# Optimization experiments

Hardware: AMD Instinct MI355X
Metric: run time of the kernel (lower is better)

## Reference

```python
import jax, jax.numpy as jnp
import numpy as np

N_NODES = 50000
N_EDGES = 1600000
NUM_GRAPHS = 512
NEG_SLOPE = 0.2


def _glorot(key, shape):
    fan_in, fan_out = shape[0], shape[-1]
    lim = jnp.sqrt(6.0 / (fan_in + fan_out))
    return jax.random.uniform(key, shape, jnp.float32, -lim, lim)


def setup_inputs() -> dict:
    key = jax.random.key(0)
    ks = jax.random.split(key, 10)
    x = jax.random.normal(ks[0], (N_NODES, 133), jnp.float32)
    edge_index = jax.random.randint(ks[1], (2, N_EDGES), 0, N_NODES, jnp.int64)
    batch = jnp.sort(jax.random.randint(ks[2], (N_NODES,), 0, NUM_GRAPHS, jnp.int64))
    # conv1: GATConv(133 -> 8, heads=8, concat=True)
    W1 = _glorot(ks[3], (133, 64))
    att_src1 = _glorot(ks[4], (8, 8))   # [H, C]
    att_dst1 = _glorot(ks[5], (8, 8))
    b1 = jnp.zeros((64,), jnp.float32)
    # conv2: GATConv(64 -> 2, heads=1, concat=True)
    W2 = _glorot(ks[6], (64, 2))
    att_src2 = _glorot(ks[7], (1, 2))
    att_dst2 = _glorot(ks[8], (1, 2))
    b2 = jnp.zeros((2,), jnp.float32)
    return {"x": x, "edge_index": edge_index, "batch": batch,
            "W1": W1, "att_src1": att_src1, "att_dst1": att_dst1, "b1": b1,
            "W2": W2, "att_src2": att_src2, "att_dst2": att_dst2, "b2": b2}


def gat_conv(x, src, dst, W, att_src, att_dst, bias):
    """PyG GATConv (add_self_loops already applied via src/dst), concat=True, eval mode."""
    N = x.shape[0]
    H, C = att_src.shape
    h = (x @ W).reshape(N, H, C)                      # [N, H, C]
    a_src = jnp.sum(h * att_src[None], axis=-1)       # [N, H]
    a_dst = jnp.sum(h * att_dst[None], axis=-1)       # [N, H]
    e = a_src[src] + a_dst[dst]                       # [E, H]
    e = jnp.where(e > 0, e, NEG_SLOPE * e)            # leaky_relu
    # segment softmax over incoming edges of each dst node
    e_max = jax.ops.segment_max(e, dst, num_segments=N)  # [N, H]
    e_exp = jnp.exp(e - e_max[dst])
    denom = jax.ops.segment_sum(e_exp, dst, num_segments=N)
    alpha = e_exp / jnp.maximum(denom, 1e-16)[dst]    # [E, H]
    msg = h[src] * alpha[:, :, None]                  # [E, H, C]
    out = jax.ops.segment_sum(msg, dst, num_segments=N)  # [N, H, C]
    return out.reshape(N, H * C) + bias


def reference(x, edge_index, batch, W1, att_src1, att_dst1, b1, W2, att_src2, att_dst2, b2):
    N = x.shape[0]
    loops = jnp.arange(N, dtype=edge_index.dtype)
    src = jnp.concatenate([edge_index[0], loops])
    dst = jnp.concatenate([edge_index[1], loops])
    # dropout layers are identity in eval mode
    h = gat_conv(x, src, dst, W1, att_src1, att_dst1, b1)   # [N, 64]
    h = jax.nn.elu(h)
    h = gat_conv(h, src, dst, W2, att_src2, att_dst2, b2)   # [N, 2]
    out = jax.ops.segment_sum(h, batch, num_segments=NUM_GRAPHS)  # [G, 2]
    return out
```

## Files before the change

kernel.cpp:

```cpp
#include <hip/hip_runtime.h>
#include <hip/hip_fp16.h>

#define NN 50000
#define NE 1600000
#define NG 512
#define NEG 0.2f

#define NBKT 782
#define NSB 512
#define CHUNK 3125
#define CAP 3072
#define NSLOT 32
#define NBI 9

typedef _Float16 half8 __attribute__((ext_vector_type(8)));
typedef float f32x4 __attribute__((ext_vector_type(4)));


__global__ __launch_bounds__(256) void k_init_count(const float* __restrict__ W1,
                                                    _Float16* __restrict__ W1f,
                                                    float* __restrict__ out,
                                                    const int* __restrict__ ei,
                                                    int* __restrict__ cnt) {
    if (blockIdx.x < NBI) {
        int i = blockIdx.x * 256 + threadIdx.x;
        if (i < 1280) {
            int f = i >> 6, l = i & 63;
            int kt = f >> 2, ct = f & 3;
            int g = l >> 4, c16 = l & 15;
#pragma unroll
            for (int j = 0; j < 8; ++j) {
                int k = kt * 32 + g * 8 + j;
                float v = (k < 133) ? W1[k * 64 + ct * 16 + c16] : 0.f;
                W1f[i * 8 + j] = (_Float16)v;
            }
        } else if (i < 1280 + NG * 2) {
            out[i - 1280] = 0.f;
        }
    } else {
        __shared__ int hist[NBKT];
        const int t = threadIdx.x, blk = blockIdx.x - NBI;
        for (int i = t; i < NBKT; i += 256) hist[i] = 0;
        __syncthreads();
        const int estart = blk * CHUNK;
        for (int e = estart + t; e < estart + CHUNK; e += 256)
            atomicAdd(&hist[ei[NE + e] >> 6], 1);
        __syncthreads();
        for (int i = t; i < NBKT; i += 256) cnt[blk * NBKT + i] = hist[i];
    }
}

__global__ __launch_bounds__(256) void k_linmfma(const float* __restrict__ x,
                                                 const _Float16* __restrict__ W1f,
                                                 const float* __restrict__ attS,
                                                 const float* __restrict__ attD,
                                                 __half* __restrict__ h1h,
                                                 float* __restrict__ aS,
                                                 float* __restrict__ aD) {
    const int wid = (blockIdx.x * 256 + threadIdx.x) >> 6;
    const int nb  = wid * 16;
    if (nb >= NN) return;
    const int l   = threadIdx.x & 63;
    const int g   = l >> 4, c16 = l & 15;
    const long xbase = (long)(nb + c16) * 133;

    half8 bfr[5][4];
#pragma unroll
    for (int kt = 0; kt < 5; ++kt)
#pragma unroll
        for (int ct = 0; ct < 4; ++ct)
            bfr[kt][ct] = *reinterpret_cast<const half8*>(W1f + ((kt * 4 + ct) * 64 + l) * 8);

    f32x4 acc[4] = {{0.f,0.f,0.f,0.f},{0.f,0.f,0.f,0.f},{0.f,0.f,0.f,0.f},{0.f,0.f,0.f,0.f}};
#pragma unroll
    for (int kt = 0; kt < 5; ++kt) {
        half8 a;
#pragma unroll
        for (int i = 0; i < 8; ++i) {
            int k = kt * 32 + g * 8 + i;
            a[i] = (_Float16)((k < 133) ? x[xbase + k] : 0.f);
        }
#pragma unroll
        for (int ct = 0; ct < 4; ++ct)
            acc[ct] = __builtin_amdgcn_mfma_f32_16x16x32_f16(a, bfr[kt][ct], acc[ct], 0, 0, 0);
    }

#pragma unroll
    for (int ct = 0; ct < 4; ++ct) {
        const int col  = ct * 16 + c16;
        const int head = col >> 3;
        const float as_w = attS[head * 8 + (col & 7)];
        const float ad_w = attD[head * 8 + (col & 7)];
#pragma unroll
        for (int r = 0; r < 4; ++r) {
            const int n = nb + g * 4 + r;
            float v = acc[ct][r];
            h1h[n * 64 + col] = __float2half(v);
            float ps = v * as_w, pd = v * ad_w;
            ps += __shfl_xor(ps, 1, 64); pd += __shfl_xor(pd, 1, 64);
            ps += __shfl_xor(ps, 2, 64); pd += __shfl_xor(pd, 2, 64);
            ps += __shfl_xor(ps, 4, 64); pd += __shfl_xor(pd, 4, 64);
            if ((l & 7) == 0) {
                aS[n * 8 + head] = ps;
                aD[n * 8 + head] = pd;
            }
        }
    }
}

__global__ __launch_bounds__(512) void k_scan(const int* __restrict__ cnt,
                                              int* __restrict__ base,
                                              int* __restrict__ tot) {
    __shared__ int s[NSB];
    const int b = blockIdx.x, t = threadIdx.x;
    int v = cnt[t * NBKT + b];
    s[t] = v;
    __syncthreads();
    for (int o = 1; o < NSB; o <<= 1) {
        int u = (t >= o) ? s[t - o] : 0;
        __syncthreads();
        s[t] += u;
        __syncthreads();
    }
    base[t * NBKT + b] = s[t] - v;
    if (t == NSB - 1) tot[b] = s[t];
}

__global__ __launch_bounds__(256) void k_place(const int* __restrict__ ei,
                                               const int* __restrict__ base,
                                               unsigned* __restrict__ binned) {
    __shared__ int hist[NBKT];
    __shared__ int basel[NBKT];
    const int t = threadIdx.x, blk = blockIdx.x;
    for (int i = t; i < NBKT; i += 256) {
        hist[i]  = 0;
        basel[i] = base[blk * NBKT + i];
    }
    __syncthreads();
    const int estart = blk * CHUNK;
    for (int e = estart + t; e < estart + CHUNK; e += 256) {
        int s = ei[e];
        int d = ei[NE + e];
        int b = d >> 6;
        int r = atomicAdd(&hist[b], 1);
        int pos = basel[b] + r;
        if (pos < CAP) binned[b * CAP + pos] = ((unsigned)s << 6) | (unsigned)(d & 63);
    }
}

__global__ __launch_bounds__(256) void k_buildcsr(const unsigned* __restrict__ binned,
                                                  const int* __restrict__ tot,
                                                  int2* __restrict__ row_se,
                                                  unsigned short* __restrict__ csr) {
    __shared__ unsigned edg[CAP];
    __shared__ unsigned short csrl[CAP];
    __shared__ int deg[64], scn[64], cur[64];

    const int b = blockIdx.x, t = threadIdx.x;
    const int ebase = b * CAP;
    const int ecnt  = min(tot[b], CAP);
    const int nbase = b << 6;
    const int ncnt  = min(64, NN - nbase);

    for (int i = t; i < ecnt; i += 256) edg[i] = binned[ebase + i];
    if (t < 64) deg[t] = 0;
    __syncthreads();
    for (int i = t; i < ecnt; i += 256) atomicAdd(&deg[edg[i] & 63], 1);
    __syncthreads();
    if (t < 64) scn[t] = deg[t];
    __syncthreads();
    for (int o = 1; o < 64; o <<= 1) {
        int v = (t < 64 && t >= o) ? scn[t - o] : 0;
        __syncthreads();
        if (t < 64) scn[t] += v;
        __syncthreads();
    }
    if (t < 64) {
        cur[t] = scn[t] - deg[t];
        if (t < ncnt) row_se[nbase + t] = make_int2(ebase + scn[t] - deg[t], ebase + scn[t]);
    }
    __syncthreads();
    for (int i = t; i < ecnt; i += 256) {
        unsigned pk = edg[i];
        int pos = atomicAdd(&cur[pk & 63], 1);
        csrl[pos] = (unsigned short)(pk >> 6);
    }
    __syncthreads();
    for (int i = t; i < ecnt; i += 256) csr[ebase + i] = csrl[i];
}

__global__ __launch_bounds__(256) void k_gather1(const unsigned short* __restrict__ csr,
                                                 const int2* __restrict__ row_se,
                                                 const float* __restrict__ aS,
                                                 const float* __restrict__ aD,
                                                 const uint2* __restrict__ h1u2,
                                                 const float* __restrict__ b1,
                                                 const float* __restrict__ W2,
                                                 const float* __restrict__ attS2,
                                                 const float* __restrict__ attD2,
                                                 float4* __restrict__ node4) {
    __shared__ float exs[4][64 * 8];
    __shared__ int   svs[4][64];

    const int sub  = threadIdx.x >> 6;
    const int lane = threadIdx.x & 63;
    const int n    = (blockIdx.x * 256 + threadIdx.x) >> 6;
    const int hp   = lane & 7;
    const int ebl  = lane >> 3;
    const int grp  = lane >> 4;
    const int c4   = lane & 15;
    const int hq   = c4 >> 1;

    const float aDhp = aD[n * 8 + hp];
    const int2 se = row_se[n];
    const int e0 = se.x, e1 = se.y;

    float ax = 0.f, ay = 0.f, az = 0.f, aw = 0.f;
    float den = 0.f;
    for (int base = e0; base < e1; base += 64) {
        const int cnt = min(64, e1 - base);
        int sv = (base + lane < e1) ? (int)csr[base + lane] : n;
        svs[sub][lane] = sv;

        const int cnt16 = (cnt + 15) & ~15;
        const int p1n   = cnt16 >> 3;

        for (int p = 0; p < p1n; ++p) {
            int eb = p * 8 + ebl;
            int s  = svs[sub][eb];
            float ev = aS[s * 8 + hp] + aDhp;
            ev = fmaxf(ev, NEG * ev);
            float ex = __expf(ev);
            if (eb >= cnt) ex = 0.f;
            exs[sub][eb * 8 + hp] = ex;
            den += ex;
        }

        for (int eb = 0; eb < cnt16; eb += 16) {
#pragma unroll
            for (int k = 0; k < 16; k += 4) {
                int   e4 = eb + k + grp;
                int   s  = svs[sub][e4];
                float ex = exs[sub][e4 * 8 + hq];
                uint2 hv = h1u2[s * 16 + c4];
                const __half2 h01 = *reinterpret_cast<const __half2*>(&hv.x);
                const __half2 h23 = *reinterpret_cast<const __half2*>(&hv.y);
                ax = fmaf(ex, __half2float(__low2half(h01)),  ax);
                ay = fmaf(ex, __half2float(__high2half(h01)), ay);
                az = fmaf(ex, __half2float(__low2half(h23)),  az);
                aw = fmaf(ex, __half2float(__high2half(h23)), aw);
            }
        }
    }
    den += __shfl_xor(den, 8, 64);
    den += __shfl_xor(den, 16, 64);
    den += __shfl_xor(den, 32, 64);
    float ev_s = aS[n * 8 + hp] + aDhp;
    ev_s = fmaxf(ev_s, NEG * ev_s);
    float ex_self = __expf(ev_s);
    den += ex_self;

    ax += __shfl_xor(ax, 16, 64); ax += __shfl_xor(ax, 32, 64);
    ay += __shfl_xor(ay, 16, 64); ay += __shfl_xor(ay, 32, 64);
    az += __shfl_xor(az, 16, 64); az += __shfl_xor(az, 32, 64);
    aw += __shfl_xor(aw, 16, 64); aw += __shfl_xor(aw, 32, 64);

    float den_q = __shfl(den, hq, 64);
    float ex_sq = __shfl(ex_self, hq, 64);

    uint2 hvs = h1u2[n * 16 + c4];
    const __half2 s01 = *reinterpret_cast<const __half2*>(&hvs.x);
    const __half2 s23 = *reinterpret_cast<const __half2*>(&hvs.y);
    float inv = 1.f / fmaxf(den_q, 1e-16f);
    float4 bb = reinterpret_cast<const float4*>(b1)[c4];
    float v0 = fmaf(ex_sq, __half2float(__low2half(s01)),  ax) * inv + bb.x;
    float v1 = fmaf(ex_sq, __half2float(__high2half(s01)), ay) * inv + bb.y;
    float v2 = fmaf(ex_sq, __half2float(__low2half(s23)),  az) * inv + bb.z;
    float v3 = fmaf(ex_sq, __half2float(__high2half(s23)), aw) * inv + bb.w;
    v0 = v0 > 0.f ? v0 : (__expf(v0) - 1.f);
    v1 = v1 > 0.f ? v1 : (__expf(v1) - 1.f);
    v2 = v2 > 0.f ? v2 : (__expf(v2) - 1.f);
    v3 = v3 > 0.f ? v3 : (__expf(v3) - 1.f);

    float4 w01 = reinterpret_cast<const float4*>(W2)[c4 * 2];
    float4 w23 = reinterpret_cast<const float4*>(W2)[c4 * 2 + 1];
    float p0 = v0 * w01.x + v1 * w01.z + v2 * w23.x + v3 * w23.z;
    float p1 = v0 * w01.y + v1 * w01.w + v2 * w23.y + v3 * w23.w;
    p0 += __shfl_xor(p0, 1, 64);  p1 += __shfl_xor(p1, 1, 64);
    p0 += __shfl_xor(p0, 2, 64);  p1 += __shfl_xor(p1, 2, 64);
    p0 += __shfl_xor(p0, 4, 64);  p1 += __shfl_xor(p1, 4, 64);
    p0 += __shfl_xor(p0, 8, 64);  p1 += __shfl_xor(p1, 8, 64);
    if (lane == 0) {
        float s2 = p0 * attS2[0] + p1 * attS2[1];
        float d2 = p0 * attD2[0] + p1 * attD2[1];
        node4[n] = make_float4(p0, p1, s2, d2);
    }
}

__global__ __launch_bounds__(256) void k_gather2(const unsigned short* __restrict__ csr,
                                                 const int2* __restrict__ row_se,
                                                 const float4* __restrict__ node4,
                                                 const int* __restrict__ batch,
                                                 const float* __restrict__ b2,
                                                 float* __restrict__ out) {
    __shared__ float pool[NSLOT][2];
    __shared__ int gbase_s;
    const int t = threadIdx.x;
    const int n = blockIdx.x * 256 + t;

    if (t == 0) gbase_s = batch[blockIdx.x * 256];
    for (int i = t; i < NSLOT * 2; i += 256) (&pool[0][0])[i] = 0.f;
    __syncthreads();

    if (n < NN) {
        const float4 vn = node4[n];
        const float aDd = vn.w;

        float ev = vn.z + aDd;
        ev = fmaxf(ev, NEG * ev);
        float ex = __expf(ev);
        float den = ex, p0 = ex * vn.x, p1 = ex * vn.y;

        const int2 se = row_se[n];
#pragma unroll 4
        for (int e = se.x; e < se.y; ++e) {
            int s = csr[e];
            float4 vs = node4[s];
            float ev2 = vs.z + aDd;
            ev2 = fmaxf(ev2, NEG * ev2);
            float ex2 = __expf(ev2);
            den += ex2;
            p0 = fmaf(ex2, vs.x, p0);
            p1 = fmaf(ex2, vs.y, p1);
        }
        float inv = 1.f / fmaxf(den, 1e-16f);
        float v0 = p0 * inv + b2[0];
        float v1 = p1 * inv + b2[1];

        int g = batch[n];
        int slot = g - gbase_s;
        if (slot < NSLOT) {
            atomicAdd(&pool[slot][0], v0);
            atomicAdd(&pool[slot][1], v1);
        } else {
            atomicAdd(&out[g * 2 + 0], v0);
            atomicAdd(&out[g * 2 + 1], v1);
        }
    }
    __syncthreads();
    for (int i = t; i < NSLOT; i += 256) {
        float v0 = pool[i][0], v1 = pool[i][1];
        if (v0 != 0.f || v1 != 0.f) {
            int g = gbase_s + i;
            atomicAdd(&out[g * 2 + 0], v0);
            atomicAdd(&out[g * 2 + 1], v1);
        }
    }
}

extern "C" void kernel_launch(void* const* d_in, const int* in_sizes, int n_in,
                              void* d_out, int out_size, void* d_ws, size_t ws_size,
                              hipStream_t stream) {
    const float* x     = (const float*)d_in[0];
    const int*   ei    = (const int*)d_in[1];
    const int*   batch = (const int*)d_in[2];
    const float* W1    = (const float*)d_in[3];
    const float* attS1 = (const float*)d_in[4];
    const float* attD1 = (const float*)d_in[5];
    const float* b1    = (const float*)d_in[6];
    const float* W2    = (const float*)d_in[7];
    const float* attS2 = (const float*)d_in[8];
    const float* attD2 = (const float*)d_in[9];
    const float* b2    = (const float*)d_in[10];
    float* out = (float*)d_out;

    int* ws = (int*)d_ws;
    __half* h1h = (__half*)ws;
    uint2* h1u2 = (uint2*)ws;
    float* aS1 = (float*)(ws + (size_t)NN * 32);
    float* aD1 = (float*)(ws + (size_t)NN * 40);
    float4* node4 = (float4*)(ws + (size_t)NN * 48);
    int2* row_se  = (int2*)(ws + (size_t)NN * 52);
    int* tot      = ws + (size_t)NN * 54;
    _Float16* W1f = (_Float16*)(ws + (size_t)NN * 54 + 1024);
    int* cnt      = ws + (size_t)NN * 55;
    int* base     = ws + (size_t)NN * 55 + (size_t)NSB * NBKT;
    unsigned* binned    = (unsigned*)(ws + (size_t)NN * 55 + 2 * (size_t)NSB * NBKT);
    unsigned short* csr = (unsigned short*)(binned + (size_t)NBKT * CAP);

    k_init_count<<<NBI + NSB, 256, 0, stream>>>(W1, W1f, out, ei, cnt);
    k_linmfma<<<(NN / 16 + 3) / 4, 256, 0, stream>>>(x, W1f, attS1, attD1, h1h, aS1, aD1);
    k_scan<<<NBKT, NSB, 0, stream>>>(cnt, base, tot);
    k_place<<<NSB, 256, 0, stream>>>(ei, base, binned);
    k_buildcsr<<<NBKT, 256, 0, stream>>>(binned, tot, row_se, csr);
    k_gather1<<<NN / 4, 256, 0, stream>>>(csr, row_se, aS1, aD1, h1u2, b1, W2,
                                          attS2, attD2, node4);
    k_gather2<<<(NN + 255) / 256, 256, 0, stream>>>(csr, row_se, node4, batch, b2, out);
}
```

Baseline: 109.5 us.

## Store layer-1 features as FP8 and merge the linear and edge-placement kernels

```diff
diff --git a/kernel.cpp b/kernel.cpp
--- a/kernel.cpp
+++ b/kernel.cpp
@@ -12,9 +12,11 @@
 #define CAP 3072
 #define NSLOT 32
 #define NBI 9
+#define NBL 782
 
 typedef _Float16 half8 __attribute__((ext_vector_type(8)));
 typedef float f32x4 __attribute__((ext_vector_type(4)));
+typedef float f32x2 __attribute__((ext_vector_type(2)));
 
 
 __global__ __launch_bounds__(256) void k_init_count(const float* __restrict__ W1,
@@ -50,64 +52,6 @@
     }
 }
 
-__global__ __launch_bounds__(256) void k_linmfma(const float* __restrict__ x,
-                                                 const _Float16* __restrict__ W1f,
-                                                 const float* __restrict__ attS,
-                                                 const float* __restrict__ attD,
-                                                 __half* __restrict__ h1h,
-                                                 float* __restrict__ aS,
-                                                 float* __restrict__ aD) {
-    const int wid = (blockIdx.x * 256 + threadIdx.x) >> 6;
-    const int nb  = wid * 16;
-    if (nb >= NN) return;
-    const int l   = threadIdx.x & 63;
-    const int g   = l >> 4, c16 = l & 15;
-    const long xbase = (long)(nb + c16) * 133;
-
-    half8 bfr[5][4];
-#pragma unroll
-    for (int kt = 0; kt < 5; ++kt)
-#pragma unroll
-        for (int ct = 0; ct < 4; ++ct)
-            bfr[kt][ct] = *reinterpret_cast<const half8*>(W1f + ((kt * 4 + ct) * 64 + l) * 8);
-
-    f32x4 acc[4] = {{0.f,0.f,0.f,0.f},{0.f,0.f,0.f,0.f},{0.f,0.f,0.f,0.f},{0.f,0.f,0.f,0.f}};
-#pragma unroll
-    for (int kt = 0; kt < 5; ++kt) {
-        half8 a;
-#pragma unroll
-        for (int i = 0; i < 8; ++i) {
-            int k = kt * 32 + g * 8 + i;
-            a[i] = (_Float16)((k < 133) ? x[xbase + k] : 0.f);
-        }
-#pragma unroll
-        for (int ct = 0; ct < 4; ++ct)
-            acc[ct] = __builtin_amdgcn_mfma_f32_16x16x32_f16(a, bfr[kt][ct], acc[ct], 0, 0, 0);
-    }
-
-#pragma unroll
-    for (int ct = 0; ct < 4; ++ct) {
-        const int col  = ct * 16 + c16;
-        const int head = col >> 3;
-        const float as_w = attS[head * 8 + (col & 7)];
-        const float ad_w = attD[head * 8 + (col & 7)];
-#pragma unroll
-        for (int r = 0; r < 4; ++r) {
-            const int n = nb + g * 4 + r;
-            float v = acc[ct][r];
-            h1h[n * 64 + col] = __float2half(v);
-            float ps = v * as_w, pd = v * ad_w;
-            ps += __shfl_xor(ps, 1, 64); pd += __shfl_xor(pd, 1, 64);
-            ps += __shfl_xor(ps, 2, 64); pd += __shfl_xor(pd, 2, 64);
-            ps += __shfl_xor(ps, 4, 64); pd += __shfl_xor(pd, 4, 64);
-            if ((l & 7) == 0) {
-                aS[n * 8 + head] = ps;
-                aD[n * 8 + head] = pd;
-            }
-        }
-    }
-}
-
 __global__ __launch_bounds__(512) void k_scan(const int* __restrict__ cnt,
                                               int* __restrict__ base,
                                               int* __restrict__ tot) {
@@ -126,25 +70,85 @@
     if (t == NSB - 1) tot[b] = s[t];
 }
 
-__global__ __launch_bounds__(256) void k_place(const int* __restrict__ ei,
-                                               const int* __restrict__ base,
-                                               unsigned* __restrict__ binned) {
-    __shared__ int hist[NBKT];
-    __shared__ int basel[NBKT];
-    const int t = threadIdx.x, blk = blockIdx.x;
-    for (int i = t; i < NBKT; i += 256) {
-        hist[i]  = 0;
-        basel[i] = base[blk * NBKT + i];
-    }
-    __syncthreads();
-    const int estart = blk * CHUNK;
-    for (int e = estart + t; e < estart + CHUNK; e += 256) {
-        int s = ei[e];
-        int d = ei[NE + e];
-        int b = d >> 6;
-        int r = atomicAdd(&hist[b], 1);
-        int pos = basel[b] + r;
-        if (pos < CAP) binned[b * CAP + pos] = ((unsigned)s << 6) | (unsigned)(d & 63);
+__global__ __launch_bounds__(256) void k_lin_place(const float* __restrict__ x,
+                                                   const _Float16* __restrict__ W1f,
+                                                   const float* __restrict__ attS,
+                                                   const float* __restrict__ attD,
+                                                   unsigned char* __restrict__ h1b,
+                                                   float* __restrict__ aS,
+                                                   float* __restrict__ aD,
+                                                   const int* __restrict__ ei,
+                                                   const int* __restrict__ base,
+                                                   unsigned* __restrict__ binned) {
+    if (blockIdx.x < NBL) {
+        const int wid = (blockIdx.x * 256 + threadIdx.x) >> 6;
+        const int nb  = wid * 16;
+        if (nb >= NN) return;
+        const int l   = threadIdx.x & 63;
+        const int g   = l >> 4, c16 = l & 15;
+        const long xbase = (long)(nb + c16) * 133;
+
+        half8 bfr[5][4];
+#pragma unroll
+        for (int kt = 0; kt < 5; ++kt)
+#pragma unroll
+            for (int ct = 0; ct < 4; ++ct)
+                bfr[kt][ct] = *reinterpret_cast<const half8*>(W1f + ((kt * 4 + ct) * 64 + l) * 8);
+
+        f32x4 acc[4] = {{0.f,0.f,0.f,0.f},{0.f,0.f,0.f,0.f},{0.f,0.f,0.f,0.f},{0.f,0.f,0.f,0.f}};
+#pragma unroll
+        for (int kt = 0; kt < 5; ++kt) {
+            half8 a;
+#pragma unroll
+            for (int i = 0; i < 8; ++i) {
+                int k = kt * 32 + g * 8 + i;
+                a[i] = (_Float16)((k < 133) ? x[xbase + k] : 0.f);
+            }
+#pragma unroll
+            for (int ct = 0; ct < 4; ++ct)
+                acc[ct] = __builtin_amdgcn_mfma_f32_16x16x32_f16(a, bfr[kt][ct], acc[ct], 0, 0, 0);
+        }
+
+#pragma unroll
+        for (int ct = 0; ct < 4; ++ct) {
+            const int col  = ct * 16 + c16;
+            const int head = col >> 3;
+            const float as_w = attS[head * 8 + (col & 7)];
+            const float ad_w = attD[head * 8 + (col & 7)];
+#pragma unroll
+            for (int r = 0; r < 4; ++r) {
+                const int n = nb + g * 4 + r;
+                float v = acc[ct][r];
+                h1b[n * 64 + col] =
+                    (unsigned char)__builtin_amdgcn_cvt_pk_fp8_f32(v, v, 0, false);
+                float ps = v * as_w, pd = v * ad_w;
+                ps += __shfl_xor(ps, 1, 64); pd += __shfl_xor(pd, 1, 64);
+                ps += __shfl_xor(ps, 2, 64); pd += __shfl_xor(pd, 2, 64);
+                ps += __shfl_xor(ps, 4, 64); pd += __shfl_xor(pd, 4, 64);
+                if ((l & 7) == 0) {
+                    aS[n * 8 + head] = ps;
+                    aD[n * 8 + head] = pd;
+                }
+            }
+        }
+    } else {
+        __shared__ int hist[NBKT];
+        __shared__ int basel[NBKT];
+        const int t = threadIdx.x, blk = blockIdx.x - NBL;
+        for (int i = t; i < NBKT; i += 256) {
+            hist[i]  = 0;
+            basel[i] = base[blk * NBKT + i];
+        }
+        __syncthreads();
+        const int estart = blk * CHUNK;
+        for (int e = estart + t; e < estart + CHUNK; e += 256) {
+            int s = ei[e];
+            int d = ei[NE + e];
+            int b = d >> 6;
+            int r = atomicAdd(&hist[b], 1);
+            int pos = basel[b] + r;
+            if (pos < CAP) binned[b * CAP + pos] = ((unsigned)s << 6) | (unsigned)(d & 63);
+        }
     }
 }
 
@@ -193,7 +197,7 @@
                                                  const int2* __restrict__ row_se,
                                                  const float* __restrict__ aS,
                                                  const float* __restrict__ aD,
-                                                 const uint2* __restrict__ h1u2,
+                                                 const unsigned* __restrict__ h1w,
                                                  const float* __restrict__ b1,
                                                  const float* __restrict__ W2,
                                                  const float* __restrict__ attS2,
@@ -242,13 +246,13 @@
                 int   e4 = eb + k + grp;
                 int   s  = svs[sub][e4];
                 float ex = exs[sub][e4 * 8 + hq];
-                uint2 hv = h1u2[s * 16 + c4];
-                const __half2 h01 = *reinterpret_cast<const __half2*>(&hv.x);
-                const __half2 h23 = *reinterpret_cast<const __half2*>(&hv.y);
-                ax = fmaf(ex, __half2float(__low2half(h01)),  ax);
-                ay = fmaf(ex, __half2float(__high2half(h01)), ay);
-                az = fmaf(ex, __half2float(__low2half(h23)),  az);
-                aw = fmaf(ex, __half2float(__high2half(h23)), aw);
+                unsigned hv = h1w[s * 16 + c4];
+                f32x2 f01 = __builtin_amdgcn_cvt_pk_f32_fp8(hv, false);
+                f32x2 f23 = __builtin_amdgcn_cvt_pk_f32_fp8(hv, true);
+                ax = fmaf(ex, f01.x, ax);
+                ay = fmaf(ex, f01.y, ay);
+                az = fmaf(ex, f23.x, az);
+                aw = fmaf(ex, f23.y, aw);
             }
         }
     }
@@ -268,15 +272,15 @@
     float den_q = __shfl(den, hq, 64);
     float ex_sq = __shfl(ex_self, hq, 64);
 
-    uint2 hvs = h1u2[n * 16 + c4];
-    const __half2 s01 = *reinterpret_cast<const __half2*>(&hvs.x);
-    const __half2 s23 = *reinterpret_cast<const __half2*>(&hvs.y);
+    unsigned hvs = h1w[n * 16 + c4];
+    f32x2 s01 = __builtin_amdgcn_cvt_pk_f32_fp8(hvs, false);
+    f32x2 s23 = __builtin_amdgcn_cvt_pk_f32_fp8(hvs, true);
     float inv = 1.f / fmaxf(den_q, 1e-16f);
     float4 bb = reinterpret_cast<const float4*>(b1)[c4];
-    float v0 = fmaf(ex_sq, __half2float(__low2half(s01)),  ax) * inv + bb.x;
-    float v1 = fmaf(ex_sq, __half2float(__high2half(s01)), ay) * inv + bb.y;
-    float v2 = fmaf(ex_sq, __half2float(__low2half(s23)),  az) * inv + bb.z;
-    float v3 = fmaf(ex_sq, __half2float(__high2half(s23)), aw) * inv + bb.w;
+    float v0 = fmaf(ex_sq, s01.x, ax) * inv + bb.x;
+    float v1 = fmaf(ex_sq, s01.y, ay) * inv + bb.y;
+    float v2 = fmaf(ex_sq, s23.x, az) * inv + bb.z;
+    float v3 = fmaf(ex_sq, s23.y, aw) * inv + bb.w;
     v0 = v0 > 0.f ? v0 : (__expf(v0) - 1.f);
     v1 = v1 > 0.f ? v1 : (__expf(v1) - 1.f);
     v2 = v2 > 0.f ? v2 : (__expf(v2) - 1.f);
@@ -375,8 +379,8 @@
     float* out = (float*)d_out;
 
     int* ws = (int*)d_ws;
-    __half* h1h = (__half*)ws;
-    uint2* h1u2 = (uint2*)ws;
+    unsigned char* h1b = (unsigned char*)ws;
+    unsigned* h1w = (unsigned*)ws;
     float* aS1 = (float*)(ws + (size_t)NN * 32);
     float* aD1 = (float*)(ws + (size_t)NN * 40);
     float4* node4 = (float4*)(ws + (size_t)NN * 48);
@@ -389,11 +393,11 @@
     unsigned short* csr = (unsigned short*)(binned + (size_t)NBKT * CAP);
 
     k_init_count<<<NBI + NSB, 256, 0, stream>>>(W1, W1f, out, ei, cnt);
-    k_linmfma<<<(NN / 16 + 3) / 4, 256, 0, stream>>>(x, W1f, attS1, attD1, h1h, aS1, aD1);
     k_scan<<<NBKT, NSB, 0, stream>>>(cnt, base, tot);
-    k_place<<<NSB, 256, 0, stream>>>(ei, base, binned);
+    k_lin_place<<<NBL + NSB, 256, 0, stream>>>(x, W1f, attS1, attD1, h1b, aS1, aD1,
+                                               ei, base, binned);
     k_buildcsr<<<NBKT, 256, 0, stream>>>(binned, tot, row_se, csr);
-    k_gather1<<<NN / 4, 256, 0, stream>>>(csr, row_se, aS1, aD1, h1u2, b1, W2,
+    k_gather1<<<NN / 4, 256, 0, stream>>>(csr, row_se, aS1, aD1, h1w, b1, W2,
                                           attS2, attD2, node4);
     k_gather2<<<(NN + 255) / 256, 256, 0, stream>>>(csr, row_se, node4, batch, b2, out);
 }
```

New measurement: 102.3 us. 6.6% less time.
